# Kernel optimization log

Hardware: AMD Instinct MI355X
Metric: run time of the kernel (lower is better)

Reference implementation:

```python
import jax, jax.numpy as jnp
import numpy as np

EPS = 1e-5
KS = 3
PAD = 1


def _bn(x, g, b, m, v):
    inv = g / jnp.sqrt(v + EPS)
    return x * inv[None, :, None, None] + (b - m * inv)[None, :, None, None]


def _deform_conv2d(x, off_w, off_b, w):
    # x: (B,C,H,W); off_w: (2*9,C,3,3); w: (Cout,C,3,3)
    B, C, H, W = x.shape
    N = KS * KS
    off = jax.lax.conv_general_dilated(x, off_w, (1, 1), ((PAD, PAD), (PAD, PAD)))
    off = off + off_b[None, :, None, None]                      # (B,2N,H,W)
    xp = jnp.pad(x, ((0, 0), (0, 0), (PAD, PAD), (PAD, PAD)))
    Hp, Wp = H + 2 * PAD, W + 2 * PAD
    r = jnp.arange(KS, dtype=x.dtype) - (KS - 1) // 2           # kernel offsets
    pny = jnp.repeat(r, KS)                                     # row-major (dy)
    pnx = jnp.tile(r, KS)                                       # row-major (dx)
    p0y = jnp.arange(1, H + 1, dtype=x.dtype)[None, None, :, None]
    p0x = jnp.arange(1, W + 1, dtype=x.dtype)[None, None, None, :]
    py = off[:, :N] + pny[None, :, None, None] + p0y            # (B,N,H,W)
    px = off[:, N:] + pnx[None, :, None, None] + p0x
    py = jnp.clip(py, 0.0, Hp - 1.0)
    px = jnp.clip(px, 0.0, Wp - 1.0)
    fy = jax.lax.stop_gradient(jnp.floor(py))                   # indices detached (as in torch impl)
    fx = jax.lax.stop_gradient(jnp.floor(px))
    qy0 = jnp.clip(fy, 0.0, Hp - 1.0)
    qx0 = jnp.clip(fx, 0.0, Wp - 1.0)
    qy1 = jnp.clip(fy + 1.0, 0.0, Hp - 1.0)
    qx1 = jnp.clip(fx + 1.0, 0.0, Wp - 1.0)
    xf = xp.reshape(B, C, Hp * Wp)

    def gather(qy, qx):
        idx = (qy * Wp + qx).astype(jnp.int32)                  # (B,N,H,W)
        return jax.vmap(lambda m_, i_: m_[:, i_])(xf, idx)       # (B,C,N,H,W)

    g_lt = (1.0 + (qy0 - py)) * (1.0 + (qx0 - px))
    g_rb = (1.0 - (qy1 - py)) * (1.0 - (qx1 - px))
    g_lb = (1.0 + (qy0 - py)) * (1.0 - (qx1 - px))
    g_rt = (1.0 - (qy1 - py)) * (1.0 + (qx0 - px))
    xo = (g_lt[:, None] * gather(qy0, qx0) + g_rb[:, None] * gather(qy1, qx1)
          + g_lb[:, None] * gather(qy0, qx1) + g_rt[:, None] * gather(qy1, qx0))
    # (B,C,N,H,W) -> (B,C,H*KS,W*KS): N = (row, col) row-major
    xo = xo.reshape(B, C, KS, KS, H, W).transpose(0, 1, 4, 2, 5, 3).reshape(B, C, H * KS, W * KS)
    return jax.lax.conv_general_dilated(xo, w, (KS, KS), 'VALID')


def _forward(x, dc1_offw, dc1_offb, dc1_w, bn1_g, bn1_b, bn1_m, bn1_v,
             dc2_offw, dc2_offb, dc2_w, bn2_g, bn2_b, bn2_m, bn2_v,
             id_w, id_b, bn3_g, bn3_b, bn3_m, bn3_v):
    h = jax.nn.relu(_bn(_deform_conv2d(x, dc1_offw, dc1_offb, dc1_w), bn1_g, bn1_b, bn1_m, bn1_v))
    h = _bn(_deform_conv2d(h, dc2_offw, dc2_offb, dc2_w), bn2_g, bn2_b, bn2_m, bn2_v)
    idt = jnp.einsum('bchw,oc->bohw', x, id_w[:, :, 0, 0]) + id_b[None, :, None, None]
    idt = _bn(idt, bn3_g, bn3_b, bn3_m, bn3_v)
    return jax.nn.relu(h + idt)


def setup_inputs() -> dict:
    key = jax.random.key(0)
    ks = jax.random.split(key, 16)
    B, Cin, Cout, H, W = 2, 64, 128, 128, 128
    N2 = 2 * KS * KS
    d = {}
    d['x'] = jax.random.normal(ks[0], (B, Cin, H, W), jnp.float32)
    d['dc1_offw'] = jax.random.normal(ks[1], (N2, Cin, KS, KS), jnp.float32) * 0.01
    d['dc1_offb'] = jnp.zeros((N2,), jnp.float32)
    d['dc1_w'] = jax.random.normal(ks[2], (Cout, Cin, KS, KS), jnp.float32) * 0.05
    d['bn1_g'] = 1.0 + 0.1 * jax.random.normal(ks[3], (Cout,), jnp.float32)
    d['bn1_b'] = 0.1 * jax.random.normal(ks[4], (Cout,), jnp.float32)
    d['bn1_m'] = 0.1 * jax.random.normal(ks[5], (Cout,), jnp.float32)
    d['bn1_v'] = jnp.ones((Cout,), jnp.float32)
    d['dc2_offw'] = jax.random.normal(ks[6], (N2, Cout, KS, KS), jnp.float32) * 0.01
    d['dc2_offb'] = jnp.zeros((N2,), jnp.float32)
    d['dc2_w'] = jax.random.normal(ks[7], (Cout, Cout, KS, KS), jnp.float32) * 0.03
    d['bn2_g'] = 1.0 + 0.1 * jax.random.normal(ks[8], (Cout,), jnp.float32)
    d['bn2_b'] = 0.1 * jax.random.normal(ks[9], (Cout,), jnp.float32)
    d['bn2_m'] = 0.1 * jax.random.normal(ks[10], (Cout,), jnp.float32)
    d['bn2_v'] = jnp.ones((Cout,), jnp.float32)
    d['id_w'] = jax.random.normal(ks[11], (Cout, Cin, 1, 1), jnp.float32) * 0.1
    d['id_b'] = jnp.zeros((Cout,), jnp.float32)
    d['bn3_g'] = 1.0 + 0.1 * jax.random.normal(ks[12], (Cout,), jnp.float32)
    d['bn3_b'] = 0.1 * jax.random.normal(ks[13], (Cout,), jnp.float32)
    d['bn3_m'] = 0.1 * jax.random.normal(ks[14], (Cout,), jnp.float32)
    d['bn3_v'] = jnp.ones((Cout,), jnp.float32)
    return d


def reference(x, dc1_offw, dc1_offb, dc1_w, bn1_g, bn1_b, bn1_m, bn1_v,
              dc2_offw, dc2_offb, dc2_w, bn2_g, bn2_b, bn2_m, bn2_v,
              id_w, id_b, bn3_g, bn3_b, bn3_m, bn3_v):
    return _forward(x, dc1_offw, dc1_offb, dc1_w, bn1_g, bn1_b, bn1_m, bn1_v,
                    dc2_offw, dc2_offb, dc2_w, bn2_g, bn2_b, bn2_m, bn2_v,
                    id_w, id_b, bn3_g, bn3_b, bn3_m, bn3_v)
```

## Files before the change

kernel.cpp:

```cpp
#include <hip/hip_runtime.h>
#include <math.h>

#define HH 128
#define WW 128
#define HWSZ (HH * WW)
#define BB 2
#define COUT 128

typedef __bf16 bf16x8 __attribute__((ext_vector_type(8)));
typedef float f32x4 __attribute__((ext_vector_type(4)));
typedef float f32x2 __attribute__((ext_vector_type(2)));
typedef short s16x8 __attribute__((ext_vector_type(8)));
typedef short s16x4 __attribute__((ext_vector_type(4)));
typedef unsigned short u16x4 __attribute__((ext_vector_type(4)));
typedef unsigned short u16x8 __attribute__((ext_vector_type(8)));

__device__ __forceinline__ short tobf(float f) {
  union { float f; unsigned u; } v; v.f = f;
  unsigned r = v.u + 0x7fffu + ((v.u >> 16) & 1u);
  return (short)(r >> 16);
}
__device__ __forceinline__ float asf(unsigned u) {
  union { unsigned u; float f; } v; v.u = u;
  return v.f;
}
__device__ __forceinline__ f32x2 up2(unsigned u) {
  f32x2 r; r[0] = asf(u << 16); r[1] = asf(u & 0xffff0000u); return r;
}
__device__ __forceinline__ unsigned trunc2bf(f32x2 v) {
  union { float f; unsigned u; } a, b;
  a.f = v[0]; b.f = v[1];
  return __builtin_amdgcn_perm(b.u, a.u, 0x07060302u);
}

#define PA0 73728
#define PA1 221184
#define PA2 229376
#define PA3 247808
#define PA4 284672
#define PA5 284928
__global__ __launch_bounds__(256) void prep_all_kernel(
    const float* __restrict__ dc1_w, const float* __restrict__ dc2_w,
    const float* __restrict__ id_w, const float* __restrict__ dc1_offw,
    const float* __restrict__ dc2_offw,
    const float* g1, const float* b1, const float* m1, const float* v1,
    const float* g2, const float* b2, const float* m2, const float* v2,
    const float* g3, const float* b3, const float* m3, const float* v3,
    const float* idb,
    short* __restrict__ wbf1, short* __restrict__ wbf2,
    short* __restrict__ woff1, short* __restrict__ woff2,
    float* __restrict__ cb1, float* __restrict__ cb2) {
  int idx = blockIdx.x * 256 + threadIdx.x;
  if (idx < PA0) {
    int o = idx / 576, k = idx - o * 576;
    float inv = g1[o] / sqrtf(v1[o] + 1e-5f);
    int col = (k % 9) * 64 + k / 9;
    int di = (((col >> 5) * 2 + (o >> 6)) * 4 + ((o >> 4) & 3)) * 512
           + (((o & 15) | (((col >> 3) & 3) << 4)) * 8) + (col & 7);
    wbf1[di] = tobf(dc1_w[(size_t)o * 576 + k] * inv);
  } else if (idx < PA1) {
    int j = idx - PA0;
    int o = j / 1152, k = j - o * 1152;
    float inv = g2[o] / sqrtf(v2[o] + 1e-5f);
    int col = (k % 9) * 128 + k / 9;
    int di = (((col >> 5) * 2 + (o >> 6)) * 4 + ((o >> 4) & 3)) * 512
           + (((o & 15) | (((col >> 3) & 3) << 4)) * 8) + (col & 7);
    wbf2[di] = tobf(dc2_w[(size_t)o * 1152 + k] * inv);
  } else if (idx < PA2) {
    int j = idx - PA1;
    int o = j >> 6, k = j & 63;
    float inv = g3[o] / sqrtf(v3[o] + 1e-5f);
    int col = 1152 + k;
    int di = (((col >> 5) * 2 + (o >> 6)) * 4 + ((o >> 4) & 3)) * 512
           + (((o & 15) | (((col >> 3) & 3) << 4)) * 8) + (col & 7);
    wbf2[di] = tobf(id_w[(size_t)o * 64 + k] * inv);
  } else if (idx < PA3) {
    int j = idx - PA2;
    int o = j / 576, k = j - o * 576;
    int col = (k % 9) * 64 + k / 9;
    int di = ((col >> 5) * 2 + (o >> 4)) * 512 + ((col >> 3) & 3) * 128
           + (o & 15) * 8 + (col & 7);
    woff1[di] = (o < 18) ? tobf(dc1_offw[(size_t)o * 576 + k]) : (short)0;
  } else if (idx < PA4) {
    int j = idx - PA3;
    int o = j / 1152, k = j - o * 1152;
    int col = (k % 9) * 128 + k / 9;
    int di = ((col >> 5) * 2 + (o >> 4)) * 512 + ((col >> 3) & 3) * 128
           + (o & 15) * 8 + (col & 7);
    woff2[di] = (o < 18) ? tobf(dc2_offw[(size_t)o * 1152 + k]) : (short)0;
  } else if (idx < PA5) {
    int j = idx - PA4;
    if (j < 128) {
      float inv = g1[j] / sqrtf(v1[j] + 1e-5f);
      cb1[j] = b1[j] - m1[j] * inv;
    } else {
      int o = j - 128;
      float inv2_ = g2[o] / sqrtf(v2[o] + 1e-5f);
      float inv3_ = g3[o] / sqrtf(v3[o] + 1e-5f);
      cb2[o] = (b2[o] - m2[o] * inv2_) + idb[o] * inv3_ + (b3[o] - m3[o] * inv3_);
    }
  }
}

__global__ __launch_bounds__(256) void xcast_kernel(const float* __restrict__ x,
                                                    unsigned short* __restrict__ xn) {
  __shared__ short lds[64 * 72];
  int tid = threadIdx.x;
  int gp0 = blockIdx.x * 64;
  int b = gp0 >> 14;
  int pl0 = gp0 & 16383;
  int p = tid & 63;
  int cb = (tid >> 6) * 16;
#pragma unroll
  for (int i = 0; i < 16; i++) {
    int c = cb + i;
    lds[p * 72 + c] = tobf(x[((size_t)(b * 64 + c)) * HWSZ + pl0 + p]);
  }
  __syncthreads();
  int pw = tid >> 2, cseg = (tid & 3) * 16;
  u16x8 a = *(const u16x8*)&lds[pw * 72 + cseg];
  u16x8 b8 = *(const u16x8*)&lds[pw * 72 + cseg + 8];
  *(u16x8*)&xn[(size_t)(gp0 + pw) * 64 + cseg] = a;
  *(u16x8*)&xn[(size_t)(gp0 + pw) * 64 + cseg + 8] = b8;
}

template <int CSH>
__global__ __launch_bounds__(512, 4) void offconv_mfma_kernel(
    const unsigned short* __restrict__ in, const short* __restrict__ woff,
    const float* __restrict__ offb, float* __restrict__ off) {
  __shared__ float redf[4 * 64 * 8];
  constexpr int Cin = 1 << CSH;
  constexpr int HK = (9 << CSH) >> 1;
  constexpr int NCh = HK >> 5;
  const int tid = threadIdx.x;
  const int lane = tid & 63, wv = tid >> 6;
  const int pxg = wv & 3, kh = wv >> 2;
  const int pb = ((blockIdx.x & 7) << 6) | (blockIdx.x >> 3);
  const int pix0 = pb << 6;
  const int x0 = pix0 & 127, y = (pix0 >> 7) & 127, b = pix0 >> 14;
  const unsigned short* inb = in + (size_t)b * HWSZ * Cin;
  const int l15 = lane & 15, quad = lane >> 4;
  const int px = x0 + pxg * 16 + l15;

  f32x4 acc[2];
  acc[0] = (f32x4){0.f, 0.f, 0.f, 0.f};
  acc[1] = (f32x4){0.f, 0.f, 0.f, 0.f};

#pragma unroll
  for (int i = 0; i < NCh; i++) {
    int k0 = kh * HK + i * 32;
    int n = k0 >> CSH;
    int c0 = (k0 & (Cin - 1)) + quad * 8;
    int yy = y + n / 3 - 1;
    int xx = px + n % 3 - 1;
    bf16x8 bv = {};
    if (((unsigned)yy < (unsigned)HH) && ((unsigned)xx < (unsigned)WW))
      bv = *(const bf16x8*)&inb[((size_t)yy * WW + xx) * Cin + c0];
    int fbase = (k0 >> 5) * 1024 + lane * 8;
    bf16x8 a0 = *(const bf16x8*)&woff[fbase];
    bf16x8 a1 = *(const bf16x8*)&woff[fbase + 512];
    acc[0] = __builtin_amdgcn_mfma_f32_16x16x32_bf16(a0, bv, acc[0], 0, 0, 0);
    acc[1] = __builtin_amdgcn_mfma_f32_16x16x32_bf16(a1, bv, acc[1], 0, 0, 0);
  }
  if (kh == 1) {
    *(f32x4*)&redf[(pxg * 64 + lane) * 8] = acc[0];
    *(f32x4*)&redf[(pxg * 64 + lane) * 8 + 4] = acc[1];
  }
  __syncthreads();
  if (kh == 0) {
    acc[0] += *(const f32x4*)&redf[(pxg * 64 + lane) * 8];
    acc[1] += *(const f32x4*)&redf[(pxg * 64 + lane) * 8 + 4];
#pragma unroll
    for (int ot = 0; ot < 2; ot++) {
#pragma unroll
      for (int r = 0; r < 4; r++) {
        int o = ot * 16 + quad * 4 + r;
        if (o < 18)
          off[(size_t)(b * 18 + o) * HWSZ + y * WW + px] = acc[ot][r] + offb[o];
      }
    }
  }
}

#define LOADW(P, kc_)                                           \
  {                                                             \
    const short* wf_ = wfb + (size_t)(kc_) * 4096;              \
    P##w0 = *(const bf16x8*)(wf_);                              \
    P##w1 = *(const bf16x8*)(wf_ + 512);                        \
    P##w2 = *(const bf16x8*)(wf_ + 1024);                       \
    P##w3 = *(const bf16x8*)(wf_ + 1536);                       \
    P##w4 = *(const bf16x8*)(wf_ + 2048);                       \
    P##w5 = *(const bf16x8*)(wf_ + 2560);                       \
    P##w6 = *(const bf16x8*)(wf_ + 3072);                       \
    P##w7 = *(const bf16x8*)(wf_ + 3584);                       \
  }

#define LOADT(P, kc_)                                           \
  {                                                             \
    int k0_ = (kc_) << 5;                                       \
    int n_ = k0_ >> CSH;                                        \
    int c0_ = (k0_ & (Cin - 1)) + cq * 8;                       \
    uint4 d4_ = dsu[(n_ << 6) + dp0];                           \
    int dx_ = (int)(d4_.w & 0xffffu);                           \
    int dy_ = (int)d4_.w >> 16;                                 \
    const unsigned short* p_ = inb + (int)d4_.z + c0_;          \
    P##q00 = *(const uint4*)(p_);                               \
    P##q01 = *(const uint4*)(p_ + dx_);                         \
    P##q02 = *(const uint4*)(p_ + dy_);                         \
    P##q03 = *(const uint4*)(p_ + dx_ + dy_);                   \
    P##wa0 = d4_.x; P##wb0 = d4_.y;                             \
    uint4 e4_ = dsu[(n_ << 6) + dp1];                           \
    int ex_ = (int)(e4_.w & 0xffffu);                           \
    int ey_ = (int)e4_.w >> 16;                                 \
    const unsigned short* q_ = inb + (int)e4_.z + c0_;          \
    P##q10 = *(const uint4*)(q_);                               \
    P##q11 = *(const uint4*)(q_ + ex_);                         \
    P##q12 = *(const uint4*)(q_ + ey_);                         \
    P##q13 = *(const uint4*)(q_ + ex_ + ey_);                   \
    P##wa1 = e4_.x; P##wb1 = e4_.y;                             \
  }

#define BLEND1(r0, r1, r2, r3, wav, wbv, pkv)                                 \
  {                                                                           \
    float w0_ = asf((wav) << 16), w1_ = asf((wav) & 0xffff0000u);             \
    float w2_ = asf((wbv) << 16), w3_ = asf((wbv) & 0xffff0000u);             \
    f32x2 v0_ = up2(r0.x) * w0_ + up2(r1.x) * w1_                             \
              + up2(r2.x) * w2_ + up2(r3.x) * w3_;                            \
    f32x2 v1_ = up2(r0.y) * w0_ + up2(r1.y) * w1_                             \
              + up2(r2.y) * w2_ + up2(r3.y) * w3_;                            \
    f32x2 v2_ = up2(r0.z) * w0_ + up2(r1.z) * w1_                             \
              + up2(r2.z) * w2_ + up2(r3.z) * w3_;                            \
    f32x2 v3_ = up2(r0.w) * w0_ + up2(r1.w) * w1_                             \
              + up2(r2.w) * w2_ + up2(r3.w) * w3_;                            \
    pkv.x = trunc2bf(v0_); pkv.y = trunc2bf(v1_);                             \
    pkv.z = trunc2bf(v2_); pkv.w = trunc2bf(v3_);                             \
  }

#define XPOSE(pkv, bfrv)                                                      \
  {                                                                           \
    union { int i[4]; bf16x8 v; } bu_;                                        \
    bu_.i[0] = __builtin_amdgcn_ds_bpermute(baddr, (int)pkv.x);               \
    bu_.i[1] = __builtin_amdgcn_ds_bpermute(baddr, (int)pkv.y);               \
    bu_.i[2] = __builtin_amdgcn_ds_bpermute(baddr, (int)pkv.z);               \
    bu_.i[3] = __builtin_amdgcn_ds_bpermute(baddr, (int)pkv.w);               \
    bfrv = bu_.v;                                                             \
  }

#define MFMA16(P, bfr0v, bfr1v)                                                     \
  {                                                                                 \
    acc[0] = __builtin_amdgcn_mfma_f32_16x16x32_bf16(P##w0, bfr0v, acc[0], 0, 0, 0);  \
    acc[8] = __builtin_amdgcn_mfma_f32_16x16x32_bf16(P##w0, bfr1v, acc[8], 0, 0, 0);  \
    acc[1] = __builtin_amdgcn_mfma_f32_16x16x32_bf16(P##w1, bfr0v, acc[1], 0, 0, 0);  \
    acc[9] = __builtin_amdgcn_mfma_f32_16x16x32_bf16(P##w1, bfr1v, acc[9], 0, 0, 0);  \
    acc[2] = __builtin_amdgcn_mfma_f32_16x16x32_bf16(P##w2, bfr0v, acc[2], 0, 0, 0);  \
    acc[10] = __builtin_amdgcn_mfma_f32_16x16x32_bf16(P##w2, bfr1v, acc[10], 0, 0, 0);\
    acc[3] = __builtin_amdgcn_mfma_f32_16x16x32_bf16(P##w3, bfr0v, acc[3], 0, 0, 0);  \
    acc[11] = __builtin_amdgcn_mfma_f32_16x16x32_bf16(P##w3, bfr1v, acc[11], 0, 0, 0);\
    acc[4] = __builtin_amdgcn_mfma_f32_16x16x32_bf16(P##w4, bfr0v, acc[4], 0, 0, 0);  \
    acc[12] = __builtin_amdgcn_mfma_f32_16x16x32_bf16(P##w4, bfr1v, acc[12], 0, 0, 0);\
    acc[5] = __builtin_amdgcn_mfma_f32_16x16x32_bf16(P##w5, bfr0v, acc[5], 0, 0, 0);  \
    acc[13] = __builtin_amdgcn_mfma_f32_16x16x32_bf16(P##w5, bfr1v, acc[13], 0, 0, 0);\
    acc[6] = __builtin_amdgcn_mfma_f32_16x16x32_bf16(P##w6, bfr0v, acc[6], 0, 0, 0);  \
    acc[14] = __builtin_amdgcn_mfma_f32_16x16x32_bf16(P##w6, bfr1v, acc[14], 0, 0, 0);\
    acc[7] = __builtin_amdgcn_mfma_f32_16x16x32_bf16(P##w7, bfr0v, acc[7], 0, 0, 0);  \
    acc[15] = __builtin_amdgcn_mfma_f32_16x16x32_bf16(P##w7, bfr1v, acc[15], 0, 0, 0);\
  }

#define COMPUTE(P)                                                            \
  {                                                                           \
    uint4 pk0_, pk1_;                                                         \
    BLEND1(P##q00, P##q01, P##q02, P##q03, P##wa0, P##wb0, pk0_);             \
    BLEND1(P##q10, P##q11, P##q12, P##q13, P##wa1, P##wb1, pk1_);             \
    bf16x8 bf0_, bf1_;                                                        \
    XPOSE(pk0_, bf0_);                                                        \
    XPOSE(pk1_, bf1_);                                                        \
    MFMA16(P, bf0_, bf1_);                                                    \
  }

template <int CSH, int KCONV, int KTOT, int MODE>
__global__ __launch_bounds__(256, 2) void deform_mfma_kernel(
    const unsigned short* __restrict__ in, const float* __restrict__ off,
    const short* __restrict__ wbf, const float* __restrict__ cbv,
    const unsigned short* __restrict__ xid, float* __restrict__ outf,
    unsigned short* __restrict__ outb) {
  __shared__ __align__(16) char smem[50176];
  uint4* dsu = (uint4*)smem;
  f32x4* redf = (f32x4*)smem;
  short* trans = (short*)(smem + 32768);

  const int tid = threadIdx.x;
  const int lane = tid & 63, wv = tid >> 6;
  const int pb = ((blockIdx.x & 7) << 6) | (blockIdx.x >> 3);
  const int pix0 = pb << 6;
  const int x0 = pix0 & 127, y = (pix0 >> 7) & 127, b = pix0 >> 14;
  constexpr int Cin = 1 << CSH;
  const unsigned short* inb = in + (size_t)b * HWSZ * Cin;
  const int l15 = lane & 15, quad = lane >> 4;
  const int pxg = wv & 1, kh = wv >> 1;
  const int dp0 = pxg * 32 + (lane >> 2);
  const int dp1 = dp0 + 16;
  const int cq = lane & 3;
  const int baddr = (((lane & 15) << 2) | (lane >> 4)) << 2;

  constexpr int NC = KTOT >> 5;
  constexpr int NCONV = KCONV >> 5;
  constexpr int HC = NC >> 1;
  const int kcBeg = kh * HC;
  const int kcEnd = kcBeg + HC;
  const int kcEndConv = (kcEnd < NCONV) ? kcEnd : NCONV;
  const short* wfb = wbf + lane * 8;

  bf16x8 Aw0, Aw1, Aw2, Aw3, Aw4, Aw5, Aw6, Aw7;
  bf16x8 Bw0, Bw1, Bw2, Bw3, Bw4, Bw5, Bw6, Bw7;
  uint4 Aq00, Aq01, Aq02, Aq03, Aq10, Aq11, Aq12, Aq13;
  uint4 Bq00, Bq01, Bq02, Bq03, Bq10, Bq11, Bq12, Bq13;
  unsigned Awa0, Awb0, Awa1, Awb1, Bwa0, Bwb0, Bwa1, Bwb1;

  LOADW(A, kcBeg);

  for (int t = tid; t < 576; t += 256) {
    int n = t >> 6, pp = t & 63;
    float offy = off[(size_t)(b * 18 + n) * HWSZ + y * WW + x0 + pp];
    float offx = off[(size_t)(b * 18 + 9 + n) * HWSZ + y * WW + x0 + pp];
    float py = offy + (float)(n / 3 - 1) + (float)(y + 1);
    float px = offx + (float)(n % 3 - 1) + (float)(x0 + pp + 1);
    py = fminf(fmaxf(py, 0.f), 129.f);
    px = fminf(fmaxf(px, 0.f), 129.f);
    float fy = floorf(py), fx = floorf(px);
    float qy1 = fminf(fy + 1.f, 129.f), qx1 = fminf(fx + 1.f, 129.f);
    float ty0 = 1.f + fy - py, ty1 = 1.f - (qy1 - py);
    float tx0 = 1.f + fx - px, tx1 = 1.f - (qx1 - px);
    int iy0 = (int)fy - 1, ix0 = (int)fx - 1;
    int iy1 = (int)qy1 - 1, ix1 = (int)qx1 - 1;
    if ((unsigned)iy0 >= (unsigned)HH) ty0 = 0.f;
    if ((unsigned)iy1 >= (unsigned)HH) ty1 = 0.f;
    if ((unsigned)ix0 >= (unsigned)WW) tx0 = 0.f;
    if ((unsigned)ix1 >= (unsigned)WW) tx1 = 0.f;
    int by0 = min(max(iy0, 0), HH - 1), by1 = min(max(iy1, 0), HH - 1);
    int bx0 = min(max(ix0, 0), WW - 1), bx1 = min(max(ix1, 0), WW - 1);
    uint4 d4;
    d4.x = (unsigned)(unsigned short)tobf(ty0 * tx0)
         | ((unsigned)(unsigned short)tobf(ty0 * tx1) << 16);
    d4.y = (unsigned)(unsigned short)tobf(ty1 * tx0)
         | ((unsigned)(unsigned short)tobf(ty1 * tx1) << 16);
    d4.z = (unsigned)((by0 * WW + bx0) * Cin);
    d4.w = (unsigned)((((by1 - by0) * WW * Cin) << 16) | ((bx1 - bx0) * Cin));
    dsu[t] = d4;
  }

  f32x4 acc[16];
#pragma unroll
  for (int j = 0; j < 16; j++) acc[j] = (f32x4){0.f, 0.f, 0.f, 0.f};

  __syncthreads();

  LOADT(A, kcBeg);
  int i = kcBeg;
  for (; i + 2 <= kcEndConv; i += 2) {
    LOADW(B, i + 1);
    LOADT(B, i + 1);
    COMPUTE(A);
    if (i + 2 < kcEndConv) {
      LOADW(A, i + 2);
      LOADT(A, i + 2);
    }
    COMPUTE(B);
  }
  if (i < kcEndConv) {
    COMPUTE(A);
    i++;
  }

  if (KCONV < KTOT) {
    for (; i < kcEnd; i++) {
      LOADW(A, i);
      int c = ((i << 5) - KCONV) + cq * 8;
      uint4 pk0 = *(const uint4*)&xid[((size_t)(b * HWSZ) + y * WW + x0 + dp0) * 64 + c];
      uint4 pk1 = *(const uint4*)&xid[((size_t)(b * HWSZ) + y * WW + x0 + dp1) * 64 + c];
      bf16x8 bf0, bf1;
      XPOSE(pk0, bf0);
      XPOSE(pk1, bf1);
      MFMA16(A, bf0, bf1);
    }
  }

  __syncthreads();
  if (kh == 1) {
#pragma unroll
    for (int f = 0; f < 16; f++) redf[f * 128 + pxg * 64 + lane] = acc[f];
  }
  __syncthreads();
  if (kh == 0) {
#pragma unroll
    for (int f = 0; f < 16; f++) acc[f] += redf[f * 128 + pxg * 64 + lane];
    if (MODE == 1) {
#pragma unroll
      for (int f = 0; f < 16; f++) {
        int px_ = x0 + pxg * 32 + (f >> 3) * 16 + l15;
        int fo = f & 7;
#pragma unroll
        for (int r = 0; r < 4; r++) {
          int o = (fo >> 2) * 64 + (fo & 3) * 16 + quad * 4 + r;
          outf[(size_t)(b * COUT + o) * HWSZ + y * WW + px_] =
              fmaxf(acc[f][r] + cbv[o], 0.f);
        }
      }
    } else {
#pragma unroll
      for (int f = 0; f < 16; f++) {
        int pl = pxg * 32 + (f >> 3) * 16 + l15;
        int fo = f & 7;
        s16x4 t4;
#pragma unroll
        for (int r = 0; r < 4; r++) {
          int o = (fo >> 2) * 64 + (fo & 3) * 16 + quad * 4 + r;
          t4[r] = tobf(fmaxf(acc[f][r] + cbv[o], 0.f));
        }
        *(s16x4*)&trans[pl * 136 + (fo >> 2) * 64 + (fo & 3) * 16 + quad * 4] = t4;
      }
    }
  }
  if (MODE == 0) {
    __syncthreads();
    int pw = tid >> 2, cs = (tid & 3) * 32;
    size_t gb = ((size_t)(b * HWSZ) + y * WW + x0 + pw) * 128 + cs;
#pragma unroll
    for (int s = 0; s < 4; s++) {
      u16x8 v8 = *(const u16x8*)&trans[pw * 136 + cs + s * 8];
      *(u16x8*)&outb[gb + s * 8] = v8;
    }
  }
}

extern "C" void kernel_launch(void* const* d_in, const int* in_sizes, int n_in,
                              void* d_out, int out_size, void* d_ws, size_t ws_size,
                              hipStream_t stream) {
  const float* x        = (const float*)d_in[0];
  const float* dc1_offw = (const float*)d_in[1];
  const float* dc1_offb = (const float*)d_in[2];
  const float* dc1_w    = (const float*)d_in[3];
  const float* bn1_g    = (const float*)d_in[4];
  const float* bn1_b    = (const float*)d_in[5];
  const float* bn1_m    = (const float*)d_in[6];
  const float* bn1_v    = (const float*)d_in[7];
  const float* dc2_offw = (const float*)d_in[8];
  const float* dc2_offb = (const float*)d_in[9];
  const float* dc2_w    = (const float*)d_in[10];
  const float* bn2_g    = (const float*)d_in[11];
  const float* bn2_b    = (const float*)d_in[12];
  const float* bn2_m    = (const float*)d_in[13];
  const float* bn2_v    = (const float*)d_in[14];
  const float* id_w     = (const float*)d_in[15];
  const float* id_b     = (const float*)d_in[16];
  const float* bn3_g    = (const float*)d_in[17];
  const float* bn3_b    = (const float*)d_in[18];
  const float* bn3_m    = (const float*)d_in[19];
  const float* bn3_v    = (const float*)d_in[20];

  float* wsf = (float*)d_ws;
  float* off1 = wsf;
  float* off2 = off1 + (size_t)BB * 18 * HWSZ;
  float* cb1  = off2 + (size_t)BB * 18 * HWSZ;
  float* cb2  = cb1 + 128;
  unsigned short* xbf = (unsigned short*)(cb2 + 128);
  unsigned short* h1  = xbf + (size_t)BB * HWSZ * 64;
  short* wbf1  = (short*)(h1 + (size_t)BB * HWSZ * COUT);
  short* wbf2  = wbf1 + (size_t)128 * 576;
  short* woff1 = wbf2 + (size_t)128 * 1216;
  short* woff2 = woff1 + (size_t)18 * 1024;

  hipLaunchKernelGGL(prep_all_kernel, dim3((PA5 + 255) / 256), dim3(256), 0, stream,
                     dc1_w, dc2_w, id_w, dc1_offw, dc2_offw,
                     bn1_g, bn1_b, bn1_m, bn1_v, bn2_g, bn2_b, bn2_m, bn2_v,
                     bn3_g, bn3_b, bn3_m, bn3_v, id_b,
                     wbf1, wbf2, woff1, woff2, cb1, cb2);
  hipLaunchKernelGGL(xcast_kernel, dim3(BB * HWSZ / 64), dim3(256), 0, stream, x, xbf);

  hipLaunchKernelGGL((offconv_mfma_kernel<6>), dim3(512), dim3(512), 0, stream,
                     xbf, woff1, dc1_offb, off1);
  hipLaunchKernelGGL((deform_mfma_kernel<6, 576, 576, 0>), dim3(512), dim3(256), 0, stream,
                     xbf, off1, wbf1, cb1, (const unsigned short*)nullptr,
                     (float*)nullptr, h1);
  hipLaunchKernelGGL((offconv_mfma_kernel<7>), dim3(512), dim3(512), 0, stream,
                     h1, woff2, dc2_offb, off2);
  hipLaunchKernelGGL((deform_mfma_kernel<7, 1152, 1216, 1>), dim3(512), dim3(256), 0, stream,
                     h1, off2, wbf2, cb2, xbf, (float*)d_out,
                     (unsigned short*)nullptr);
}
```

Before: 178.0 us.

## Fuse offset convolution into deformable conv kernel via shared memory

Computes the 18-channel offset convolution inside the deformable conv kernel for its own 64-pixel tile and stores the offsets in shared memory rather than global memory. This drops two kernel launches and the global round trip of the offset tensors. In exchange, each block now runs the offset MFMA loop serially over its 4 waves (no K split), which lengthens the per-block critical path and may add register pressure. It also adds a barrier before the bilinear setup.

New measurement: 172.4 us. -3.1%, faster.

```diff
diff --git a/kernel.cpp b/kernel.cpp
--- a/kernel.cpp
+++ b/kernel.cpp
@@ -124,64 +124,6 @@
   *(u16x8*)&xn[(size_t)(gp0 + pw) * 64 + cseg + 8] = b8;
 }
 
-template <int CSH>
-__global__ __launch_bounds__(512, 4) void offconv_mfma_kernel(
-    const unsigned short* __restrict__ in, const short* __restrict__ woff,
-    const float* __restrict__ offb, float* __restrict__ off) {
-  __shared__ float redf[4 * 64 * 8];
-  constexpr int Cin = 1 << CSH;
-  constexpr int HK = (9 << CSH) >> 1;
-  constexpr int NCh = HK >> 5;
-  const int tid = threadIdx.x;
-  const int lane = tid & 63, wv = tid >> 6;
-  const int pxg = wv & 3, kh = wv >> 2;
-  const int pb = ((blockIdx.x & 7) << 6) | (blockIdx.x >> 3);
-  const int pix0 = pb << 6;
-  const int x0 = pix0 & 127, y = (pix0 >> 7) & 127, b = pix0 >> 14;
-  const unsigned short* inb = in + (size_t)b * HWSZ * Cin;
-  const int l15 = lane & 15, quad = lane >> 4;
-  const int px = x0 + pxg * 16 + l15;
-
-  f32x4 acc[2];
-  acc[0] = (f32x4){0.f, 0.f, 0.f, 0.f};
-  acc[1] = (f32x4){0.f, 0.f, 0.f, 0.f};
-
-#pragma unroll
-  for (int i = 0; i < NCh; i++) {
-    int k0 = kh * HK + i * 32;
-    int n = k0 >> CSH;
-    int c0 = (k0 & (Cin - 1)) + quad * 8;
-    int yy = y + n / 3 - 1;
-    int xx = px + n % 3 - 1;
-    bf16x8 bv = {};
-    if (((unsigned)yy < (unsigned)HH) && ((unsigned)xx < (unsigned)WW))
-      bv = *(const bf16x8*)&inb[((size_t)yy * WW + xx) * Cin + c0];
-    int fbase = (k0 >> 5) * 1024 + lane * 8;
-    bf16x8 a0 = *(const bf16x8*)&woff[fbase];
-    bf16x8 a1 = *(const bf16x8*)&woff[fbase + 512];
-    acc[0] = __builtin_amdgcn_mfma_f32_16x16x32_bf16(a0, bv, acc[0], 0, 0, 0);
-    acc[1] = __builtin_amdgcn_mfma_f32_16x16x32_bf16(a1, bv, acc[1], 0, 0, 0);
-  }
-  if (kh == 1) {
-    *(f32x4*)&redf[(pxg * 64 + lane) * 8] = acc[0];
-    *(f32x4*)&redf[(pxg * 64 + lane) * 8 + 4] = acc[1];
-  }
-  __syncthreads();
-  if (kh == 0) {
-    acc[0] += *(const f32x4*)&redf[(pxg * 64 + lane) * 8];
-    acc[1] += *(const f32x4*)&redf[(pxg * 64 + lane) * 8 + 4];
-#pragma unroll
-    for (int ot = 0; ot < 2; ot++) {
-#pragma unroll
-      for (int r = 0; r < 4; r++) {
-        int o = ot * 16 + quad * 4 + r;
-        if (o < 18)
-          off[(size_t)(b * 18 + o) * HWSZ + y * WW + px] = acc[ot][r] + offb[o];
-      }
-    }
-  }
-}
-
 #define LOADW(P, kc_)                                           \
   {                                                             \
     const short* wf_ = wfb + (size_t)(kc_) * 4096;              \
@@ -278,14 +220,16 @@
   }
 
 template <int CSH, int KCONV, int KTOT, int MODE>
-__global__ __launch_bounds__(256, 2) void deform_mfma_kernel(
-    const unsigned short* __restrict__ in, const float* __restrict__ off,
+__global__ __launch_bounds__(256, 2) void fused_layer_kernel(
+    const unsigned short* __restrict__ in, const short* __restrict__ woff,
+    const float* __restrict__ offb,
     const short* __restrict__ wbf, const float* __restrict__ cbv,
     const unsigned short* __restrict__ xid, float* __restrict__ outf,
     unsigned short* __restrict__ outb) {
   __shared__ __align__(16) char smem[50176];
   uint4* dsu = (uint4*)smem;
   f32x4* redf = (f32x4*)smem;
+  float* offlds = (float*)(smem + 32768);
   short* trans = (short*)(smem + 32768);
 
   const int tid = threadIdx.x;
@@ -302,6 +246,44 @@
   const int cq = lane & 3;
   const int baddr = (((lane & 15) << 2) | (lane >> 4)) << 2;
 
+  {
+    constexpr int NCh = (9 << CSH) >> 5;
+    const int pxa = wv;
+    const int px = x0 + pxa * 16 + l15;
+    f32x4 aco0 = {0.f, 0.f, 0.f, 0.f};
+    f32x4 aco1 = {0.f, 0.f, 0.f, 0.f};
+#pragma unroll
+    for (int i = 0; i < NCh; i++) {
+      int k0 = i * 32;
+      int n = k0 >> CSH;
+      int c0 = (k0 & (Cin - 1)) + quad * 8;
+      int yy = y + n / 3 - 1;
+      int xx = px + n % 3 - 1;
+      bf16x8 bv = {};
+      if (((unsigned)yy < (unsigned)HH) && ((unsigned)xx < (unsigned)WW))
+        bv = *(const bf16x8*)&inb[((size_t)yy * WW + xx) * Cin + c0];
+      int fbase = i * 1024 + lane * 8;
+      bf16x8 a0 = *(const bf16x8*)&woff[fbase];
+      bf16x8 a1 = *(const bf16x8*)&woff[fbase + 512];
+      aco0 = __builtin_amdgcn_mfma_f32_16x16x32_bf16(a0, bv, aco0, 0, 0, 0);
+      aco1 = __builtin_amdgcn_mfma_f32_16x16x32_bf16(a1, bv, aco1, 0, 0, 0);
+    }
+#pragma unroll
+    for (int r = 0; r < 4; r++) {
+      int o0 = quad * 4 + r;
+      offlds[o0 * 64 + pxa * 16 + l15] = aco0[r] + offb[o0];
+      int o1 = 16 + quad * 4 + r;
+      if (o1 < 18)
+        offlds[o1 * 64 + pxa * 16 + l15] = aco1[r] + offb[o1];
+    }
+  }
+
+  bf16x8 Aw0, Aw1, Aw2, Aw3, Aw4, Aw5, Aw6, Aw7;
+  bf16x8 Bw0, Bw1, Bw2, Bw3, Bw4, Bw5, Bw6, Bw7;
+  uint4 Aq00, Aq01, Aq02, Aq03, Aq10, Aq11, Aq12, Aq13;
+  uint4 Bq00, Bq01, Bq02, Bq03, Bq10, Bq11, Bq12, Bq13;
+  unsigned Awa0, Awb0, Awa1, Awb1, Bwa0, Bwb0, Bwa1, Bwb1;
+
   constexpr int NC = KTOT >> 5;
   constexpr int NCONV = KCONV >> 5;
   constexpr int HC = NC >> 1;
@@ -310,18 +292,13 @@
   const int kcEndConv = (kcEnd < NCONV) ? kcEnd : NCONV;
   const short* wfb = wbf + lane * 8;
 
-  bf16x8 Aw0, Aw1, Aw2, Aw3, Aw4, Aw5, Aw6, Aw7;
-  bf16x8 Bw0, Bw1, Bw2, Bw3, Bw4, Bw5, Bw6, Bw7;
-  uint4 Aq00, Aq01, Aq02, Aq03, Aq10, Aq11, Aq12, Aq13;
-  uint4 Bq00, Bq01, Bq02, Bq03, Bq10, Bq11, Bq12, Bq13;
-  unsigned Awa0, Awb0, Awa1, Awb1, Bwa0, Bwb0, Bwa1, Bwb1;
-
   LOADW(A, kcBeg);
+  __syncthreads();
 
   for (int t = tid; t < 576; t += 256) {
     int n = t >> 6, pp = t & 63;
-    float offy = off[(size_t)(b * 18 + n) * HWSZ + y * WW + x0 + pp];
-    float offx = off[(size_t)(b * 18 + 9 + n) * HWSZ + y * WW + x0 + pp];
+    float offy = offlds[n * 64 + pp];
+    float offx = offlds[(9 + n) * 64 + pp];
     float py = offy + (float)(n / 3 - 1) + (float)(y + 1);
     float px = offx + (float)(n % 3 - 1) + (float)(x0 + pp + 1);
     py = fminf(fmaxf(py, 0.f), 129.f);
@@ -458,9 +435,7 @@
   const float* bn3_v    = (const float*)d_in[20];
 
   float* wsf = (float*)d_ws;
-  float* off1 = wsf;
-  float* off2 = off1 + (size_t)BB * 18 * HWSZ;
-  float* cb1  = off2 + (size_t)BB * 18 * HWSZ;
+  float* cb1  = wsf;
   float* cb2  = cb1 + 128;
   unsigned short* xbf = (unsigned short*)(cb2 + 128);
   unsigned short* h1  = xbf + (size_t)BB * HWSZ * 64;
@@ -476,14 +451,10 @@
                      wbf1, wbf2, woff1, woff2, cb1, cb2);
   hipLaunchKernelGGL(xcast_kernel, dim3(BB * HWSZ / 64), dim3(256), 0, stream, x, xbf);
 
-  hipLaunchKernelGGL((offconv_mfma_kernel<6>), dim3(512), dim3(512), 0, stream,
-                     xbf, woff1, dc1_offb, off1);
-  hipLaunchKernelGGL((deform_mfma_kernel<6, 576, 576, 0>), dim3(512), dim3(256), 0, stream,
-                     xbf, off1, wbf1, cb1, (const unsigned short*)nullptr,
-                     (float*)nullptr, h1);
-  hipLaunchKernelGGL((offconv_mfma_kernel<7>), dim3(512), dim3(512), 0, stream,
-                     h1, woff2, dc2_offb, off2);
-  hipLaunchKernelGGL((deform_mfma_kernel<7, 1152, 1216, 1>), dim3(512), dim3(256), 0, stream,
-                     h1, off2, wbf2, cb2, xbf, (float*)d_out,
-                     (unsigned short*)nullptr);
-}
+  hipLaunchKernelGGL((fused_layer_kernel<6, 576, 576, 0>), dim3(512), dim3(256), 0, stream,
+                     xbf, woff1, dc1_offb, wbf1, cb1,
+                     (const unsigned short*)nullptr, (float*)nullptr, h1);
+  hipLaunchKernelGGL((fused_layer_kernel<7, 1152, 1216, 1>), dim3(512), dim3(256), 0, stream,
+                     h1, woff2, dc2_offb, wbf2, cb2,
+                     xbf, (float*)d_out, (unsigned short*)nullptr);
+}
```
